# Optimization experiments

Hardware: AMD Instinct MI355X
Metric: run time of the kernel (lower is better)

The kernel has to match this reference:

```python
import jax, jax.numpy as jnp
import numpy as np

PATCH = 14
MERGE = 2
HIDDEN = 1024
# (H, W) in pixels; all multiples of PATCH with even patch grids (divisible by MERGE)
IMAGE_SIZES = np.array([[1540, 1540], [1120, 1540], [1540, 896], [784, 1260],
                        [1512, 1512], [1540, 1120], [896, 896], [1260, 1540]], dtype=np.int64)


def setup_inputs() -> dict:
    key = jax.random.key(0)
    k1, k2 = jax.random.split(key)
    sizes_p = IMAGE_SIZES // PATCH
    total_tokens = int((sizes_p[:, 0] * sizes_p[:, 1]).sum())  # 67440
    image_features = jax.random.normal(k1, (total_tokens, HIDDEN), dtype=jnp.float32)
    # nn.Linear(hidden*merge**2 -> hidden, bias=False): weight shape [out, in] = [1024, 4096]
    merging_weight = jax.random.normal(k2, (HIDDEN, HIDDEN * MERGE * MERGE), dtype=jnp.float32) * 0.02
    image_sizes = jnp.asarray(IMAGE_SIZES)
    return {"image_features": image_features, "merging_weight": merging_weight, "image_sizes": image_sizes}


def _merge_patches(feats, sizes_np):
    """Per-image unfold(kernel=MERGE, stride=MERGE) over the [hp, wp] patch grid.
    torch unfold orders the flattened channel dim as d*m*m + ki*m + kj (channel-major),
    blocks in row-major (i, j) order -> reshape/transpose below reproduces it exactly."""
    m = MERGE
    D = feats.shape[-1]
    out, off = [], 0
    for h, w in sizes_np:  # small fixed set of images (static shapes)
        hp, wp = int(h) // PATCH, int(w) // PATCH
        n = hp * wp
        g = jax.lax.dynamic_slice_in_dim(feats, off, n, axis=0)
        g = g.reshape(hp // m, m, wp // m, m, D)          # [i, ki, j, kj, d]
        g = g.transpose(0, 2, 4, 1, 3).reshape(-1, D * m * m)  # [i*j, d*ki*kj]
        out.append(g)
        off += n
    return jnp.concatenate(out, axis=0)  # [total_tokens / m^2, D*m^2]


def reference(image_features, merging_weight, image_sizes):
    sizes_np = np.asarray(jax.device_get(image_sizes))  # static metadata
    merged = _merge_patches(image_features, sizes_np)
    return merged @ merging_weight.T  # [total/4, HIDDEN]
```

## Files before the change

kernel.cpp:

```cpp
#include <hip/hip_runtime.h>
#include <hip/hip_bf16.h>

#define MTOK  16860
#define NTOK  67440
#define NOUT  1024
#define KDIM  4096
#define NBM   132

__device__ __constant__ int c_mend[8] = {3025,5225,6985,8245,11161,13361,14385,16860};
__device__ __constant__ int c_moff[8] = {0,3025,5225,6985,8245,11161,13361,14385};
__device__ __constant__ int c_foff[8] = {0,12100,20900,27940,32980,44644,53444,57540};
__device__ __constant__ int c_wp[8]   = {110,110,64,90,108,80,64,110};

typedef __attribute__((ext_vector_type(8))) short          bf16x8;
typedef __attribute__((ext_vector_type(8))) unsigned short u16x8;
typedef __attribute__((ext_vector_type(4))) float          f32x4;

__device__ __forceinline__ unsigned short f2bf(float f) {
    unsigned int u = __float_as_uint(f);
    u += 0x7FFFu + ((u >> 16) & 1u);
    return (unsigned short)(u >> 16);
}

__device__ __forceinline__ void async_copy16(const void* g, void* l) {
    __builtin_amdgcn_global_load_lds(
        (const __attribute__((address_space(1))) void*)g,
        (__attribute__((address_space(3))) void*)l, 16, 0, 0);
}

__global__ __launch_bounds__(256) void cast_feats(const float* __restrict__ f,
                                                  unsigned short* __restrict__ o) {
    size_t g = ((size_t)blockIdx.x * 256 + threadIdx.x) * 8;
    float4 a = *(const float4*)(f + g);
    float4 b = *(const float4*)(f + g + 4);
    u16x8 v;
    v[0]=f2bf(a.x); v[1]=f2bf(a.y); v[2]=f2bf(a.z); v[3]=f2bf(a.w);
    v[4]=f2bf(b.x); v[5]=f2bf(b.y); v[6]=f2bf(b.z); v[7]=f2bf(b.w);
    *(u16x8*)(o + g) = v;
}

__global__ __launch_bounds__(256) void cast_w_perm(const float* __restrict__ W,
                                                   unsigned short* __restrict__ Wb) {
    int g = blockIdx.x * 256 + threadIdx.x;
    int n = g >> 10, d = g & 1023;
    float4 v = *(const float4*)(W + (size_t)n * 4096 + d * 4);
    unsigned short* o = Wb + (size_t)n * 4096 + d;
    o[0]    = f2bf(v.x);
    o[1024] = f2bf(v.y);
    o[2048] = f2bf(v.z);
    o[3072] = f2bf(v.w);
}

#define BM 128
#define BN 128
#define BK 32
__global__ __launch_bounds__(256) void gemm_fused(const unsigned short* __restrict__ A,
                                                  const unsigned short* __restrict__ B,
                                                  float* __restrict__ C) {
    __shared__ unsigned short lA[2][BM * BK];
    __shared__ unsigned short lB[2][BN * BK];

    const int orig    = blockIdx.y * 8 + blockIdx.x;
    const int logical = (orig & 7) * NBM + (orig >> 3);
    const int bn = logical & 7;
    const int bm = logical >> 3;

    const int tid  = threadIdx.x;
    const int wave = tid >> 6, lane = tid & 63;
    const int wm = (wave >> 1) * 64, wn = (wave & 1) * 64;

    const int lrow = lane >> 2;
    const int lcol = (lane & 3) * 8;

    int abase[2], awp[2];
#pragma unroll
    for (int r = 0; r < 2; ++r) {
        int chunk = wave * 2 + r;
        int t = bm * BM + chunk * 16 + lrow;
        if (t >= MTOK) t = 0;
        int im = 0;
        while (t >= c_mend[im]) im++;
        int rr  = t - c_moff[im];
        int wp  = c_wp[im];
        int wp2 = wp >> 1;
        int i = rr / wp2, j = rr - i * wp2;
        abase[r] = c_foff[im] + 2 * i * wp + 2 * j;
        awp[r]   = wp;
    }

    const unsigned short* Bbase = B + (size_t)bn * BN * KDIM;

    f32x4 acc[4][4];
#pragma unroll
    for (int a = 0; a < 4; ++a)
#pragma unroll
        for (int b = 0; b < 4; ++b) acc[a][b] = (f32x4){0.f, 0.f, 0.f, 0.f};

    const int mrow = lane & 15;
    const int kq   = (lane >> 4) * 8;

#pragma unroll
    for (int r = 0; r < 2; ++r) {
        int chunk = wave * 2 + r;
        int row   = chunk * 16 + lrow;
        async_copy16(A + (((size_t)abase[r]) << 10) + lcol,
                     &lA[0][chunk * 512 + lane * 8]);
        async_copy16(Bbase + (size_t)row * KDIM + lcol,
                     &lB[0][chunk * 512 + lane * 8]);
    }

    for (int k0 = 0; k0 < KDIM; k0 += BK) {
        const int cur = (k0 >> 5) & 1;
        __syncthreads();

        if (k0 + BK < KDIM) {
            const int nxt = cur ^ 1;
            const int kn  = k0 + BK;
            const int c   = kn >> 10;
            const int d0  = kn & 1023;
#pragma unroll
            for (int r = 0; r < 2; ++r) {
                int chunk = wave * 2 + r;
                int row   = chunk * 16 + lrow;
                int fr = abase[r] + ((c & 2) ? awp[r] : 0) + (c & 1);
                async_copy16(A + (((size_t)fr) << 10) + d0 + lcol,
                             &lA[nxt][chunk * 512 + lane * 8]);
                async_copy16(Bbase + (size_t)row * KDIM + kn + lcol,
                             &lB[nxt][chunk * 512 + lane * 8]);
            }
        }

        bf16x8 af[4], bfr[4];
#pragma unroll
        for (int a = 0; a < 4; ++a) {
            af[a]  = *(const bf16x8*)&lA[cur][(wm + a * 16 + mrow) * BK + kq];
            bfr[a] = *(const bf16x8*)&lB[cur][(wn + a * 16 + mrow) * BK + kq];
        }
#pragma unroll
        for (int a = 0; a < 4; ++a)
#pragma unroll
            for (int b = 0; b < 4; ++b)
                acc[a][b] = __builtin_amdgcn_mfma_f32_16x16x32_bf16(af[a], bfr[b], acc[a][b], 0, 0, 0);
    }

    const int col   = lane & 15;
    const int rquad = (lane >> 4) * 4;
#pragma unroll
    for (int a = 0; a < 4; ++a) {
        int gm0 = bm * BM + wm + a * 16 + rquad;
#pragma unroll
        for (int b = 0; b < 4; ++b) {
            int gn = bn * BN + wn + b * 16 + col;
#pragma unroll
            for (int rg = 0; rg < 4; ++rg) {
                int gm = gm0 + rg;
                if (gm < MTOK) C[(size_t)gm * NOUT + gn] = acc[a][b][rg];
            }
        }
    }
}

__global__ __launch_bounds__(256) void naive_fb(const float* __restrict__ feats,
                                                const float* __restrict__ W,
                                                float* __restrict__ out) {
    int t = blockIdx.x;
    int o = blockIdx.y * 256 + threadIdx.x;
    int im = 0;
    while (t >= c_mend[im]) im++;
    int r = t - c_moff[im];
    int wp = c_wp[im], wp2 = wp >> 1;
    int i = r / wp2, j = r - i * wp2;
    const float* f00 = feats + (size_t)(c_foff[im] + (2*i)*wp + 2*j) * 1024;
    const float* f10 = f00 + (size_t)wp * 1024;
    const float* w = W + (size_t)o * 4096;
    float s = 0.f;
    for (int d = 0; d < 1024; ++d)
        s += f00[d] * w[d*4] + f00[d+1024] * w[d*4+1] + f10[d] * w[d*4+2] + f10[d+1024] * w[d*4+3];
    out[(size_t)t * 1024 + o] = s;
}

extern "C" void kernel_launch(void* const* d_in, const int* in_sizes, int n_in,
                              void* d_out, int out_size, void* d_ws, size_t ws_size,
                              hipStream_t stream) {
    const float* feats = (const float*)d_in[0];
    const float* W     = (const float*)d_in[1];
    float* out         = (float*)d_out;

    const size_t need = ((size_t)NTOK * 1024 + (size_t)NOUT * KDIM) * sizeof(unsigned short);
    if (ws_size >= need) {
        unsigned short* featsbf = (unsigned short*)d_ws;
        unsigned short* Wb      = featsbf + (size_t)NTOK * 1024;
        cast_feats<<<dim3(NTOK * 1024 / (256 * 8)), 256, 0, stream>>>(feats, featsbf);
        cast_w_perm<<<dim3(NOUT * 1024 / 256), 256, 0, stream>>>(W, Wb);
        gemm_fused<<<dim3(NOUT / BN, NBM), 256, 0, stream>>>(featsbf, Wb, out);
    } else {
        naive_fb<<<dim3(MTOK, 4), 256, 0, stream>>>(feats, W, out);
    }
}
```

Before: 725.1 us.

## Deepen GEMM K-tile to 64 with XOR-swizzled LDS and fused cast kernels

The two cast kernels become one launch, which removes a kernel launch. The GEMM K tile grows from 32 to 64 and the LDS layout gets an XOR swizzle to avoid bank conflicts. Loads are now two stages ahead, controlled by explicit vmcnt waits and barriers, and s_setprio is raised around the MFMA block. This costs more LDS (64KB per block, with a launch bound of 2 blocks per CU). Relying on raw waitcnt values makes the code fragile if the compiler reorders loads.

After: 611.3 us. -15.7%, faster.

```diff
diff --git a/kernel.cpp b/kernel.cpp
--- a/kernel.cpp
+++ b/kernel.cpp
@@ -6,6 +6,7 @@
 #define NOUT  1024
 #define KDIM  4096
 #define NBM   132
+#define KTILES 64
 
 __device__ __constant__ int c_mend[8] = {3025,5225,6985,8245,11161,13361,14385,16860};
 __device__ __constant__ int c_moff[8] = {0,3025,5225,6985,8245,11161,13361,14385};
@@ -28,37 +29,37 @@
         (__attribute__((address_space(3))) void*)l, 16, 0, 0);
 }
 
-__global__ __launch_bounds__(256) void cast_feats(const float* __restrict__ f,
-                                                  unsigned short* __restrict__ o) {
-    size_t g = ((size_t)blockIdx.x * 256 + threadIdx.x) * 8;
-    float4 a = *(const float4*)(f + g);
-    float4 b = *(const float4*)(f + g + 4);
-    u16x8 v;
-    v[0]=f2bf(a.x); v[1]=f2bf(a.y); v[2]=f2bf(a.z); v[3]=f2bf(a.w);
-    v[4]=f2bf(b.x); v[5]=f2bf(b.y); v[6]=f2bf(b.z); v[7]=f2bf(b.w);
-    *(u16x8*)(o + g) = v;
-}
-
-__global__ __launch_bounds__(256) void cast_w_perm(const float* __restrict__ W,
-                                                   unsigned short* __restrict__ Wb) {
-    int g = blockIdx.x * 256 + threadIdx.x;
-    int n = g >> 10, d = g & 1023;
-    float4 v = *(const float4*)(W + (size_t)n * 4096 + d * 4);
-    unsigned short* o = Wb + (size_t)n * 4096 + d;
-    o[0]    = f2bf(v.x);
-    o[1024] = f2bf(v.y);
-    o[2048] = f2bf(v.z);
-    o[3072] = f2bf(v.w);
-}
-
-#define BM 128
-#define BN 128
-#define BK 32
-__global__ __launch_bounds__(256) void gemm_fused(const unsigned short* __restrict__ A,
-                                                  const unsigned short* __restrict__ B,
-                                                  float* __restrict__ C) {
-    __shared__ unsigned short lA[2][BM * BK];
-    __shared__ unsigned short lB[2][BN * BK];
+#define CF_BLOCKS 33720
+__global__ __launch_bounds__(256) void cast_all(const float* __restrict__ feats,
+                                                const float* __restrict__ W,
+                                                unsigned short* __restrict__ fb,
+                                                unsigned short* __restrict__ Wb) {
+    int b = blockIdx.x;
+    if (b < CF_BLOCKS) {
+        size_t g = ((size_t)b * 256 + threadIdx.x) * 8;
+        float4 a = *(const float4*)(feats + g);
+        float4 c = *(const float4*)(feats + g + 4);
+        u16x8 v;
+        v[0]=f2bf(a.x); v[1]=f2bf(a.y); v[2]=f2bf(a.z); v[3]=f2bf(a.w);
+        v[4]=f2bf(c.x); v[5]=f2bf(c.y); v[6]=f2bf(c.z); v[7]=f2bf(c.w);
+        *(u16x8*)(fb + g) = v;
+    } else {
+        int g = (b - CF_BLOCKS) * 256 + threadIdx.x;
+        int n = g >> 10, d = g & 1023;
+        float4 v = *(const float4*)(W + (size_t)n * 4096 + d * 4);
+        unsigned short* o = Wb + (size_t)n * 4096 + d;
+        o[0]    = f2bf(v.x);
+        o[1024] = f2bf(v.y);
+        o[2048] = f2bf(v.z);
+        o[3072] = f2bf(v.w);
+    }
+}
+
+__global__ __launch_bounds__(256, 2) void gemm_fused(const unsigned short* __restrict__ A,
+                                                     const unsigned short* __restrict__ B,
+                                                     float* __restrict__ C) {
+    __shared__ unsigned short lA[2][128 * 64];
+    __shared__ unsigned short lB[2][128 * 64];
 
     const int orig    = blockIdx.y * 8 + blockIdx.x;
     const int logical = (orig & 7) * NBM + (orig >> 3);
@@ -69,26 +70,42 @@
     const int wave = tid >> 6, lane = tid & 63;
     const int wm = (wave >> 1) * 64, wn = (wave & 1) * 64;
 
-    const int lrow = lane >> 2;
-    const int lcol = (lane & 3) * 8;
-
-    int abase[2], awp[2];
-#pragma unroll
-    for (int r = 0; r < 2; ++r) {
-        int chunk = wave * 2 + r;
-        int t = bm * BM + chunk * 16 + lrow;
+    const int srow = tid >> 3;
+    const int sp   = tid & 7;
+    const int ssw  = (sp ^ (srow & 7)) * 8;
+    const int sdst = srow * 64 + sp * 8;
+
+    int fbase[4], fwp[4];
+#pragma unroll
+    for (int i = 0; i < 4; ++i) {
+        int t = bm * 128 + i * 32 + srow;
         if (t >= MTOK) t = 0;
         int im = 0;
         while (t >= c_mend[im]) im++;
         int rr  = t - c_moff[im];
         int wp  = c_wp[im];
         int wp2 = wp >> 1;
-        int i = rr / wp2, j = rr - i * wp2;
-        abase[r] = c_foff[im] + 2 * i * wp + 2 * j;
-        awp[r]   = wp;
-    }
-
-    const unsigned short* Bbase = B + (size_t)bn * BN * KDIM;
+        int ii = rr / wp2, jj = rr - ii * wp2;
+        fbase[i] = c_foff[im] + 2 * ii * wp + 2 * jj;
+        fwp[i]   = wp;
+    }
+    const unsigned short* Bb = B + (size_t)(bn * 128) * KDIM;
+
+    auto stage = [&](int kt, int buf) {
+        const int k0 = kt * 64;
+        const int c  = k0 >> 10;
+        const int dA = (k0 & 1023) + ssw;
+#pragma unroll
+        for (int i = 0; i < 4; ++i) {
+            int fr = fbase[i] + ((c & 2) ? fwp[i] : 0) + (c & 1);
+            async_copy16(A + (((size_t)fr) << 10) + dA, &lA[buf][i * 2048 + sdst]);
+        }
+#pragma unroll
+        for (int i = 0; i < 4; ++i) {
+            async_copy16(Bb + (size_t)(i * 32 + srow) * KDIM + k0 + ssw,
+                         &lB[buf][i * 2048 + sdst]);
+        }
+    };
 
     f32x4 acc[4][4];
 #pragma unroll
@@ -97,60 +114,56 @@
         for (int b = 0; b < 4; ++b) acc[a][b] = (f32x4){0.f, 0.f, 0.f, 0.f};
 
     const int mrow = lane & 15;
-    const int kq   = (lane >> 4) * 8;
-
-#pragma unroll
-    for (int r = 0; r < 2; ++r) {
-        int chunk = wave * 2 + r;
-        int row   = chunk * 16 + lrow;
-        async_copy16(A + (((size_t)abase[r]) << 10) + lcol,
-                     &lA[0][chunk * 512 + lane * 8]);
-        async_copy16(Bbase + (size_t)row * KDIM + lcol,
-                     &lB[0][chunk * 512 + lane * 8]);
-    }
-
-    for (int k0 = 0; k0 < KDIM; k0 += BK) {
-        const int cur = (k0 >> 5) & 1;
-        __syncthreads();
-
-        if (k0 + BK < KDIM) {
-            const int nxt = cur ^ 1;
-            const int kn  = k0 + BK;
-            const int c   = kn >> 10;
-            const int d0  = kn & 1023;
-#pragma unroll
-            for (int r = 0; r < 2; ++r) {
-                int chunk = wave * 2 + r;
-                int row   = chunk * 16 + lrow;
-                int fr = abase[r] + ((c & 2) ? awp[r] : 0) + (c & 1);
-                async_copy16(A + (((size_t)fr) << 10) + d0 + lcol,
-                             &lA[nxt][chunk * 512 + lane * 8]);
-                async_copy16(Bbase + (size_t)row * KDIM + kn + lcol,
-                             &lB[nxt][chunk * 512 + lane * 8]);
+    const int q8   = (lane >> 4) * 8;
+    const int rsw  = (mrow & 7) * 8;
+
+    stage(0, 0);
+    stage(1, 1);
+
+#pragma unroll 2
+    for (int kt = 0; kt < KTILES; ++kt) {
+        const int cur = kt & 1;
+        if (kt < KTILES - 1) {
+            asm volatile("s_waitcnt vmcnt(8)" ::: "memory");
+        } else {
+            asm volatile("s_waitcnt vmcnt(0)" ::: "memory");
+        }
+        __builtin_amdgcn_s_barrier();
+        __builtin_amdgcn_sched_barrier(0);
+
+        bf16x8 af[2][4], bfr[2][4];
+#pragma unroll
+        for (int ks = 0; ks < 2; ++ks) {
+            const int col = (ks * 32 + q8) ^ rsw;
+#pragma unroll
+            for (int a = 0; a < 4; ++a) {
+                af[ks][a]  = *(const bf16x8*)&lA[cur][(wm + a * 16 + mrow) * 64 + col];
+                bfr[ks][a] = *(const bf16x8*)&lB[cur][(wn + a * 16 + mrow) * 64 + col];
             }
         }
-
-        bf16x8 af[4], bfr[4];
-#pragma unroll
-        for (int a = 0; a < 4; ++a) {
-            af[a]  = *(const bf16x8*)&lA[cur][(wm + a * 16 + mrow) * BK + kq];
-            bfr[a] = *(const bf16x8*)&lB[cur][(wn + a * 16 + mrow) * BK + kq];
-        }
-#pragma unroll
-        for (int a = 0; a < 4; ++a)
-#pragma unroll
-            for (int b = 0; b < 4; ++b)
-                acc[a][b] = __builtin_amdgcn_mfma_f32_16x16x32_bf16(af[a], bfr[b], acc[a][b], 0, 0, 0);
+        __builtin_amdgcn_s_setprio(1);
+#pragma unroll
+        for (int ks = 0; ks < 2; ++ks)
+#pragma unroll
+            for (int a = 0; a < 4; ++a)
+#pragma unroll
+                for (int b = 0; b < 4; ++b)
+                    acc[a][b] = __builtin_amdgcn_mfma_f32_16x16x32_bf16(af[ks][a], bfr[ks][b],
+                                                                        acc[a][b], 0, 0, 0);
+        __builtin_amdgcn_s_setprio(0);
+        __builtin_amdgcn_sched_barrier(0);
+        __builtin_amdgcn_s_barrier();
+        if (kt + 2 < KTILES) stage(kt + 2, cur);
     }
 
     const int col   = lane & 15;
     const int rquad = (lane >> 4) * 4;
 #pragma unroll
     for (int a = 0; a < 4; ++a) {
-        int gm0 = bm * BM + wm + a * 16 + rquad;
+        int gm0 = bm * 128 + wm + a * 16 + rquad;
 #pragma unroll
         for (int b = 0; b < 4; ++b) {
-            int gn = bn * BN + wn + b * 16 + col;
+            int gn = bn * 128 + wn + b * 16 + col;
 #pragma unroll
             for (int rg = 0; rg < 4; ++rg) {
                 int gm = gm0 + rg;
@@ -190,9 +203,8 @@
     if (ws_size >= need) {
         unsigned short* featsbf = (unsigned short*)d_ws;
         unsigned short* Wb      = featsbf + (size_t)NTOK * 1024;
-        cast_feats<<<dim3(NTOK * 1024 / (256 * 8)), 256, 0, stream>>>(feats, featsbf);
-        cast_w_perm<<<dim3(NOUT * 1024 / 256), 256, 0, stream>>>(W, Wb);
-        gemm_fused<<<dim3(NOUT / BN, NBM), 256, 0, stream>>>(featsbf, Wb, out);
+        cast_all<<<dim3(CF_BLOCKS + 4096), 256, 0, stream>>>(feats, W, featsbf, Wb);
+        gemm_fused<<<dim3(NOUT / 128, NBM), 256, 0, stream>>>(featsbf, Wb, out);
     } else {
         naive_fb<<<dim3(MTOK, 4), 256, 0, stream>>>(feats, W, out);
     }
```
